# Optimization experiments

Hardware: AMD Instinct MI355X
Metric: run time of the kernel (lower is better)

The kernel has to match this reference:

```python
import jax, jax.numpy as jnp
import numpy as np

D_MODEL = 768
N_HEADS = 12
D_K = 64
EPS = 1e-5


def setup_inputs() -> dict:
    key = jax.random.key(0)
    ks = jax.random.split(key, 12)
    B, S = 4, 2048
    Q = jax.random.normal(ks[0], (B, S, D_MODEL), dtype=jnp.float32)
    K = jax.random.normal(ks[1], (B, S, D_MODEL), dtype=jnp.float32)
    V = jax.random.normal(ks[2], (B, S, D_MODEL), dtype=jnp.float32)
    attn_mask = jax.random.randint(ks[3], (B, S, S), 0, 2).astype(bool)
    s = 1.0 / np.sqrt(D_MODEL)
    Wq = jax.random.uniform(ks[4], (D_MODEL, D_MODEL), minval=-s, maxval=s)
    bq = jnp.zeros((D_MODEL,), jnp.float32)
    Wk = jax.random.uniform(ks[5], (D_MODEL, D_MODEL), minval=-s, maxval=s)
    bk = jnp.zeros((D_MODEL,), jnp.float32)
    Wv = jax.random.uniform(ks[6], (D_MODEL, D_MODEL), minval=-s, maxval=s)
    bv = jnp.zeros((D_MODEL,), jnp.float32)
    Wo = jax.random.uniform(ks[7], (D_MODEL, D_MODEL), minval=-s, maxval=s)
    bo = jnp.zeros((D_MODEL,), jnp.float32)
    gamma = jnp.ones((D_MODEL,), jnp.float32)
    beta = jnp.zeros((D_MODEL,), jnp.float32)
    return {"Q": Q, "K": K, "V": V, "attn_mask": attn_mask,
            "Wq": Wq, "bq": bq, "Wk": Wk, "bk": bk, "Wv": Wv, "bv": bv,
            "Wo": Wo, "bo": bo, "gamma": gamma, "beta": beta}


def _mha(Q, K, V, attn_mask, Wq, bq, Wk, bk, Wv, bv, Wo, bo, gamma, beta):
    B, S, _ = Q.shape
    # projections -> [B, H, S, d]
    q = (Q @ Wq + bq).reshape(B, S, N_HEADS, D_K).transpose(0, 2, 1, 3)
    k = (K @ Wk + bk).reshape(B, S, N_HEADS, D_K).transpose(0, 2, 1, 3)
    v = (V @ Wv + bv).reshape(B, S, N_HEADS, D_K).transpose(0, 2, 1, 3)
    # scaled dot-product attention with explicit [B,H,S,S] scores
    scores = jnp.einsum("bhqd,bhkd->bhqk", q, k) / np.sqrt(D_K)
    scores = jnp.where(attn_mask[:, None, :, :], -1e9, scores)
    attn = jax.nn.softmax(scores, axis=-1)
    ctx = jnp.einsum("bhqk,bhkd->bhqd", attn, v)
    ctx = ctx.transpose(0, 2, 1, 3).reshape(B, S, N_HEADS * D_K)
    out = ctx @ Wo + bo + Q  # output projection + residual
    # LayerNorm
    mu = jnp.mean(out, axis=-1, keepdims=True)
    var = jnp.mean(jnp.square(out - mu), axis=-1, keepdims=True)
    return (out - mu) * jax.lax.rsqrt(var + EPS) * gamma + beta


def reference(Q, K, V, attn_mask, Wq, bq, Wk, bk, Wv, bv, Wo, bo, gamma, beta):
    return _mha(Q, K, V, attn_mask, Wq, bq, Wk, bk, Wv, bv, Wo, bo, gamma, beta)
```

## Files before the change

kernel.cpp:

```cpp
#include <hip/hip_runtime.h>
#include <stdint.h>

#define BB 4
#define SS 2048
#define HH 12
#define DKd 64
#define DM 768
#define MROWS (BB*SS)

typedef __bf16 bfp;
typedef bfp bf16x8 __attribute__((ext_vector_type(8)));
typedef float f32x4 __attribute__((ext_vector_type(4)));

__device__ __forceinline__ unsigned short f2bf(float f) {
  union { float f; unsigned u; } c; c.f = f;
  unsigned u = c.u;
  u += 0x7FFFu + ((u >> 16) & 1u);
  return (unsigned short)(u >> 16);
}

__device__ __forceinline__ f32x4 mfma16(bf16x8 a, bf16x8 b, f32x4 c) {
  return __builtin_amdgcn_mfma_f32_16x16x32_bf16(a, b, c, 0, 0, 0);
}

__global__ __launch_bounds__(256) void wt_kernel(
    const float* __restrict__ Wq, const float* __restrict__ Wk,
    const float* __restrict__ Wv, const float* __restrict__ Wo,
    unsigned short* __restrict__ wT) {
  __shared__ float t[32][33];
  int mtx = blockIdx.z;
  const float* W = mtx == 0 ? Wq : mtx == 1 ? Wk : mtx == 2 ? Wv : Wo;
  unsigned short* out = wT + (size_t)mtx * DM * DM;
  int n0 = blockIdx.x * 32, k0 = blockIdx.y * 32;
  int tx = threadIdx.x & 31, ty = threadIdx.x >> 5;
#pragma unroll
  for (int i = 0; i < 4; i++)
    t[ty + 8 * i][tx] = W[(size_t)(k0 + ty + 8 * i) * DM + n0 + tx];
  __syncthreads();
#pragma unroll
  for (int i = 0; i < 4; i++)
    out[(size_t)(n0 + ty + 8 * i) * DM + k0 + tx] = f2bf(t[tx][ty + 8 * i]);
}

__global__ __launch_bounds__(256) void maskpack_kernel(
    const void* __restrict__ mask, unsigned short* __restrict__ pkm) {
  __shared__ int mode;
  if (threadIdx.x == 0) {
    const unsigned* w = (const unsigned*)mask;
    bool word_like = true;
    for (int i = 0; i < 64; i++) {
      unsigned x = w[i];
      if (!(x == 0u || x == 1u || x == 0x3F800000u)) { word_like = false; break; }
    }
    mode = word_like ? 1 : 0;
  }
  __syncthreads();
  int md = mode;
  int lane = threadIdx.x & 63;
  size_t total = (size_t)BB * SS * SS;
  size_t stride = (size_t)gridDim.x * blockDim.x;
  for (size_t i = (size_t)blockIdx.x * blockDim.x + threadIdx.x; i < total; i += stride) {
    int v = md ? (((const unsigned*)mask)[i] != 0u)
               : (((const unsigned char*)mask)[i] != 0);
    unsigned long long bb = __ballot(v);
    if ((lane & 15) == 0)
      pkm[i >> 4] = (unsigned short)((bb >> lane) & 0xFFFFull);
  }
}

#define Bb 128
#define LDA 40
__global__ __launch_bounds__(256) void proj_kernel(
    const float* __restrict__ Xq, const float* __restrict__ Xk, const float* __restrict__ Xv,
    const unsigned short* __restrict__ wTall,
    const float* __restrict__ bq, const float* __restrict__ bk, const float* __restrict__ bv,
    unsigned short* __restrict__ oq, unsigned short* __restrict__ ok, unsigned short* __restrict__ ov) {
  __shared__ unsigned short Al[Bb][LDA];
  __shared__ unsigned short Bl[Bb][LDA];

  int lin = blockIdx.x + gridDim.x * (blockIdx.y + gridDim.y * blockIdx.z);
  int work = (lin & 7) * 144 + (lin >> 3);
  int z = work / 384, rem = work - z * 384;
  int xb_ = rem / 6, yb = rem - xb_ * 6;

  const float* X = z == 0 ? Xq : z == 1 ? Xk : Xv;
  const unsigned short* wT = wTall + (size_t)z * DM * DM;
  const float* bias = z == 0 ? bq : z == 1 ? bk : bv;
  unsigned short* out = z == 0 ? oq : z == 1 ? ok : ov;

  int m0 = xb_ * Bb, n0 = yb * Bb;
  int tid = threadIdx.x, lane = tid & 63, wid = tid >> 6;
  int wr = (wid >> 1) * 64, wc = (wid & 1) * 64;
  int l15 = lane & 15, l4 = lane >> 4;

  f32x4 zero = {0.f, 0.f, 0.f, 0.f};
  f32x4 acc[4][4];
#pragma unroll
  for (int m = 0; m < 4; m++)
#pragma unroll
    for (int n = 0; n < 4; n++) acc[m][n] = zero;

  for (int k0 = 0; k0 < DM; k0 += 32) {
#pragma unroll
    for (int it = 0; it < 4; it++) {
      int flat = it * 256 + tid;
      int r = flat >> 3, c4 = flat & 7;
      float4 v = *reinterpret_cast<const float4*>(&X[(size_t)(m0 + r) * DM + k0 + c4 * 4]);
      unsigned short* dst = &Al[r][c4 * 4];
      dst[0] = f2bf(v.x); dst[1] = f2bf(v.y); dst[2] = f2bf(v.z); dst[3] = f2bf(v.w);
    }
#pragma unroll
    for (int it = 0; it < 2; it++) {
      int flat = it * 256 + tid;
      int r = flat >> 2, c = flat & 3;
      *reinterpret_cast<uint4*>(&Bl[r][c * 8]) =
          *reinterpret_cast<const uint4*>(&wT[(size_t)(n0 + r) * DM + k0 + c * 8]);
    }
    __syncthreads();
    bf16x8 af[4], bfr[4];
#pragma unroll
    for (int m = 0; m < 4; m++)
      af[m] = *reinterpret_cast<const bf16x8*>(&Al[wr + m * 16 + l15][l4 * 8]);
#pragma unroll
    for (int n = 0; n < 4; n++)
      bfr[n] = *reinterpret_cast<const bf16x8*>(&Bl[wc + n * 16 + l15][l4 * 8]);
#pragma unroll
    for (int m = 0; m < 4; m++)
#pragma unroll
      for (int n = 0; n < 4; n++)
        acc[m][n] = mfma16(af[m], bfr[n], acc[m][n]);
    __syncthreads();
  }
#pragma unroll
  for (int n = 0; n < 4; n++) {
    int col = n0 + wc + n * 16 + l15;
    float bv_ = bias[col];
    int h = col >> 6, d = col & 63;
#pragma unroll
    for (int m = 0; m < 4; m++) {
      int rowb = m0 + wr + m * 16 + l4 * 4;
#pragma unroll
      for (int j = 0; j < 4; j++) {
        int row = rowb + j;
        int b = row >> 11, s = row & 2047;
        out[((size_t)((b * HH + h) * SS + s)) * DKd + d] = f2bf(acc[m][n][j] + bv_);
      }
    }
  }
}

__global__ __launch_bounds__(256) void vtrans_kernel(
    const unsigned short* __restrict__ v, unsigned short* __restrict__ vT) {
  __shared__ unsigned short t[64][65];
  int bh = blockIdx.y;
  int s0 = blockIdx.x * 64;
  const unsigned short* src = v + (size_t)bh * SS * DKd;
  unsigned short* dst = vT + (size_t)bh * DKd * SS;
  int tid = threadIdx.x;
#pragma unroll
  for (int it = 0; it < 16; it++) {
    int r = it * 4 + (tid >> 6), c = tid & 63;
    t[r][c] = src[(size_t)(s0 + r) * DKd + c];
  }
  __syncthreads();
#pragma unroll
  for (int it = 0; it < 16; it++) {
    int r = it * 4 + (tid >> 6), c = tid & 63;
    dst[(size_t)r * SS + s0 + c] = t[c][r];
  }
}

#define QT 64
#define KT 64
#define LKV 72
#define LKP 76
__global__ __launch_bounds__(256) void attn_kernel(
    const unsigned short* __restrict__ q, const unsigned short* __restrict__ k,
    const unsigned short* __restrict__ vT, const unsigned short* __restrict__ pkm,
    unsigned short* __restrict__ ctx) {
  __shared__ unsigned short kl[KT][LKV];
  __shared__ unsigned short vl[DKd][LKV];
  __shared__ unsigned short pl[QT][LKP];

  int lin = blockIdx.x + blockIdx.y * gridDim.x;
  int work = (lin & 7) * 192 + (lin >> 3);
  int bh = work >> 5;
  int q0 = (work & 31) * QT;
  int b = bh / HH, h = bh - b * HH;
  int tid = threadIdx.x, lane = tid & 63, w = tid >> 6;
  int l15 = lane & 15, l4 = lane >> 4;
  const unsigned short* qp = q + (size_t)bh * SS * DKd;
  const unsigned short* kp = k + (size_t)bh * SS * DKd;
  const unsigned short* vp = vT + (size_t)bh * DKd * SS;
  const unsigned short* pkb = pkm + (size_t)b * SS * (SS / 16);

  bf16x8 aq[2];
#pragma unroll
  for (int ks = 0; ks < 2; ks++)
    aq[ks] = *reinterpret_cast<const bf16x8*>(
        &qp[(size_t)(q0 + w * 16 + l15) * DKd + ks * 32 + l4 * 8]);

  f32x4 zero = {0.f, 0.f, 0.f, 0.f};
  f32x4 acc[4];
  float lr[4] = {0.f, 0.f, 0.f, 0.f};
#pragma unroll
  for (int dn = 0; dn < 4; dn++) acc[dn] = zero;

  const float cs = 0.125f * 1.44269504f;

  for (int kt = 0; kt < SS / KT; kt++) {
#pragma unroll
    for (int it = 0; it < 2; it++) {
      int flat = it * 256 + tid;
      int r = flat >> 3, c = flat & 7;
      *reinterpret_cast<uint4*>(&kl[r][c * 8]) =
          *reinterpret_cast<const uint4*>(&kp[(size_t)(kt * KT + r) * DKd + c * 8]);
    }
#pragma unroll
    for (int it = 0; it < 2; it++) {
      int flat = it * 256 + tid;
      int r = flat >> 3, c = flat & 7;
      *reinterpret_cast<uint4*>(&vl[r][c * 8]) =
          *reinterpret_cast<const uint4*>(&vp[(size_t)r * SS + kt * KT + c * 8]);
    }
    __syncthreads();

    f32x4 sf[4];
#pragma unroll
    for (int n = 0; n < 4; n++) sf[n] = zero;
#pragma unroll
    for (int ks = 0; ks < 2; ks++) {
#pragma unroll
      for (int n = 0; n < 4; n++) {
        bf16x8 bk_ = *reinterpret_cast<const bf16x8*>(&kl[n * 16 + l15][ks * 32 + l4 * 8]);
        sf[n] = mfma16(aq[ks], bk_, sf[n]);
      }
    }

    unsigned long long pm[4];
#pragma unroll
    for (int j = 0; j < 4; j++)
      pm[j] = *reinterpret_cast<const unsigned long long*>(
          &pkb[(size_t)(q0 + w * 16 + l4 * 4 + j) * (SS / 16) + kt * 4]);
#pragma unroll
    for (int n = 0; n < 4; n++) {
#pragma unroll
      for (int j = 0; j < 4; j++) {
        unsigned bit = (unsigned)(pm[j] >> (n * 16 + l15)) & 1u;
        float arg = bit ? -1000.0f : sf[n][j] * cs;
        float p = __builtin_amdgcn_exp2f(arg);
        sf[n][j] = p;
        lr[j] += p;
      }
    }

#pragma unroll
    for (int n = 0; n < 4; n++) {
      unsigned r01, r23;
      asm("v_cvt_pk_bf16_f32 %0, %1, %2" : "=v"(r01) : "v"(sf[n][0]), "v"(sf[n][1]));
      asm("v_cvt_pk_bf16_f32 %0, %1, %2" : "=v"(r23) : "v"(sf[n][2]), "v"(sf[n][3]));
      int col = n * 16 + l15;
      pl[w * 16 + l4 * 4 + 0][col] = (unsigned short)(r01 & 0xFFFFu);
      pl[w * 16 + l4 * 4 + 1][col] = (unsigned short)(r01 >> 16);
      pl[w * 16 + l4 * 4 + 2][col] = (unsigned short)(r23 & 0xFFFFu);
      pl[w * 16 + l4 * 4 + 3][col] = (unsigned short)(r23 >> 16);
    }

    union { uint4 u; bf16x8 v; } ap[2];
#pragma unroll
    for (int ks = 0; ks < 2; ks++) {
      uint2 lo = *reinterpret_cast<const uint2*>(&pl[w * 16 + l15][ks * 32 + l4 * 8]);
      uint2 hi = *reinterpret_cast<const uint2*>(&pl[w * 16 + l15][ks * 32 + l4 * 8 + 4]);
      ap[ks].u = make_uint4(lo.x, lo.y, hi.x, hi.y);
    }

#pragma unroll
    for (int ks = 0; ks < 2; ks++) {
#pragma unroll
      for (int dn = 0; dn < 4; dn++) {
        bf16x8 bv_ = *reinterpret_cast<const bf16x8*>(&vl[dn * 16 + l15][ks * 32 + l4 * 8]);
        acc[dn] = mfma16(ap[ks].v, bv_, acc[dn]);
      }
    }
    __syncthreads();
  }

#pragma unroll
  for (int j = 0; j < 4; j++) {
#pragma unroll
    for (int off = 1; off < 16; off <<= 1) lr[j] += __shfl_xor(lr[j], off);
    lr[j] = 1.0f / lr[j];
  }
#pragma unroll
  for (int dn = 0; dn < 4; dn++) {
#pragma unroll
    for (int j = 0; j < 4; j++) {
      int grow = b * SS + q0 + w * 16 + l4 * 4 + j;
      ctx[(size_t)grow * DM + h * 64 + dn * 16 + l15] = f2bf(acc[dn][j] * lr[j]);
    }
  }
}

__global__ __launch_bounds__(256) void oproj_kernel(
    const unsigned short* __restrict__ ctx, const unsigned short* __restrict__ wT,
    const float* __restrict__ bo, const float* __restrict__ Qin, float* __restrict__ out) {
  __shared__ unsigned short Al[Bb][LDA];
  __shared__ unsigned short Bl[Bb][LDA];

  int lin = blockIdx.x + blockIdx.y * gridDim.x;
  int work = (lin & 7) * 48 + (lin >> 3);
  int xb_ = work / 6, yb = work - xb_ * 6;
  int m0 = xb_ * Bb, n0 = yb * Bb;
  int tid = threadIdx.x, lane = tid & 63, wid = tid >> 6;
  int wr = (wid >> 1) * 64, wc = (wid & 1) * 64;
  int l15 = lane & 15, l4 = lane >> 4;

  f32x4 zero = {0.f, 0.f, 0.f, 0.f};
  f32x4 acc[4][4];
#pragma unroll
  for (int m = 0; m < 4; m++)
#pragma unroll
    for (int n = 0; n < 4; n++) acc[m][n] = zero;

  for (int k0 = 0; k0 < DM; k0 += 32) {
#pragma unroll
    for (int it = 0; it < 2; it++) {
      int flat = it * 256 + tid;
      int r = flat >> 2, c = flat & 3;
      *reinterpret_cast<uint4*>(&Al[r][c * 8]) =
          *reinterpret_cast<const uint4*>(&ctx[(size_t)(m0 + r) * DM + k0 + c * 8]);
    }
#pragma unroll
    for (int it = 0; it < 2; it++) {
      int flat = it * 256 + tid;
      int r = flat >> 2, c = flat & 3;
      *reinterpret_cast<uint4*>(&Bl[r][c * 8]) =
          *reinterpret_cast<const uint4*>(&wT[(size_t)(n0 + r) * DM + k0 + c * 8]);
    }
    __syncthreads();
    bf16x8 af[4], bfr[4];
#pragma unroll
    for (int m = 0; m < 4; m++)
      af[m] = *reinterpret_cast<const bf16x8*>(&Al[wr + m * 16 + l15][l4 * 8]);
#pragma unroll
    for (int n = 0; n < 4; n++)
      bfr[n] = *reinterpret_cast<const bf16x8*>(&Bl[wc + n * 16 + l15][l4 * 8]);
#pragma unroll
    for (int m = 0; m < 4; m++)
#pragma unroll
      for (int n = 0; n < 4; n++)
        acc[m][n] = mfma16(af[m], bfr[n], acc[m][n]);
    __syncthreads();
  }
#pragma unroll
  for (int n = 0; n < 4; n++) {
    int col = n0 + wc + n * 16 + l15;
    float bv_ = bo[col];
#pragma unroll
    for (int m = 0; m < 4; m++) {
      int rowb = m0 + wr + m * 16 + l4 * 4;
#pragma unroll
      for (int j = 0; j < 4; j++) {
        int row = rowb + j;
        out[(size_t)row * DM + col] = acc[m][n][j] + bv_ + Qin[(size_t)row * DM + col];
      }
    }
  }
}

__global__ __launch_bounds__(256) void ln_kernel(
    float* __restrict__ out, const float* __restrict__ gamma, const float* __restrict__ beta) {
  int row = blockIdx.x;
  float* p = out + (size_t)row * DM;
  int t = threadIdx.x;
  float x0 = p[t], x1 = p[t + 256], x2 = p[t + 512];
  float s = x0 + x1 + x2, s2 = x0 * x0 + x1 * x1 + x2 * x2;
#pragma unroll
  for (int off = 1; off < 64; off <<= 1) {
    s += __shfl_xor(s, off);
    s2 += __shfl_xor(s2, off);
  }
  __shared__ float red[8];
  int w = t >> 6, lane = t & 63;
  if (lane == 0) { red[w] = s; red[4 + w] = s2; }
  __syncthreads();
  s = red[0] + red[1] + red[2] + red[3];
  s2 = red[4] + red[5] + red[6] + red[7];
  float mu = s * (1.0f / DM);
  float var = s2 * (1.0f / DM) - mu * mu;
  float rs = rsqrtf(var + 1e-5f);
  p[t] = (x0 - mu) * rs * gamma[t] + beta[t];
  p[t + 256] = (x1 - mu) * rs * gamma[t + 256] + beta[t + 256];
  p[t + 512] = (x2 - mu) * rs * gamma[t + 512] + beta[t + 512];
}

extern "C" void kernel_launch(void* const* d_in, const int* in_sizes, int n_in,
                              void* d_out, int out_size, void* d_ws, size_t ws_size,
                              hipStream_t stream) {
  const float* Qin = (const float*)d_in[0];
  const float* Kin = (const float*)d_in[1];
  const float* Vin = (const float*)d_in[2];
  const void* mask = d_in[3];
  const float* Wq = (const float*)d_in[4];
  const float* bq = (const float*)d_in[5];
  const float* Wk = (const float*)d_in[6];
  const float* bk = (const float*)d_in[7];
  const float* Wv = (const float*)d_in[8];
  const float* bv = (const float*)d_in[9];
  const float* Wo = (const float*)d_in[10];
  const float* bo = (const float*)d_in[11];
  const float* gamma = (const float*)d_in[12];
  const float* beta = (const float*)d_in[13];

  char* ws = (char*)d_ws;
  unsigned short* wT  = (unsigned short*)(ws);
  unsigned short* pk  = (unsigned short*)(ws + 4718592);
  unsigned short* qb  = (unsigned short*)(ws + 6815744);
  unsigned short* kb  = (unsigned short*)(ws + 6815744 + 12582912);
  unsigned short* vb  = (unsigned short*)(ws + 6815744 + 2 * 12582912);
  unsigned short* vTb = (unsigned short*)(ws + 6815744 + 3 * 12582912);
  unsigned short* ctx = vb;

  wt_kernel<<<dim3(24, 24, 4), 256, 0, stream>>>(Wq, Wk, Wv, Wo, wT);
  maskpack_kernel<<<2048, 256, 0, stream>>>(mask, pk);
  proj_kernel<<<dim3(64, 6, 3), 256, 0, stream>>>(Qin, Kin, Vin, wT, bq, bk, bv, qb, kb, vb);
  vtrans_kernel<<<dim3(32, 48), 256, 0, stream>>>(vb, vTb);
  attn_kernel<<<dim3(32, 48), 256, 0, stream>>>(qb, kb, vTb, pk, ctx);
  oproj_kernel<<<dim3(64, 6), 256, 0, stream>>>(ctx, wT + (size_t)3 * DM * DM, bo, Qin, (float*)d_out);
  ln_kernel<<<8192, 256, 0, stream>>>((float*)d_out, gamma, beta);
}
```

Baseline: 473.3 us.

## Pre-convert inputs to bf16, use direct global-to-LDS loads, widen attention key tile

Adds a conversion kernel that turns the fp32 Q/K/V activations into bf16 once, so the projection GEMM can stream bf16 tiles with global_load_lds directly into unpadded shared memory. The output projection GEMM gets the same direct-to-LDS loads. The attention kernel doubles the key tile to 128, loading wider mask words and fusing the softmax and bf16 pack loops. This costs an extra kernel launch, an extra bf16 activation buffer to write and read, and unpadded LDS rows that may cause bank conflicts.

```diff
diff --git a/kernel.cpp b/kernel.cpp
--- a/kernel.cpp
+++ b/kernel.cpp
@@ -21,6 +21,12 @@
 
 __device__ __forceinline__ f32x4 mfma16(bf16x8 a, bf16x8 b, f32x4 c) {
   return __builtin_amdgcn_mfma_f32_16x16x32_bf16(a, b, c, 0, 0, 0);
+}
+
+__device__ __forceinline__ void gload_lds16(const void* g, void* l) {
+  __builtin_amdgcn_global_load_lds(
+      (const __attribute__((address_space(1))) unsigned int*)g,
+      (__attribute__((address_space(3))) unsigned int*)l, 16, 0, 0);
 }
 
 __global__ __launch_bounds__(256) void wt_kernel(
@@ -68,22 +74,35 @@
   }
 }
 
+__global__ __launch_bounds__(256) void cvt_kernel(
+    const float* __restrict__ Q, const float* __restrict__ K, const float* __restrict__ V,
+    unsigned short* __restrict__ xb) {
+  int z = blockIdx.z;
+  const float* src = z == 0 ? Q : z == 1 ? K : V;
+  unsigned short* dst = xb + (size_t)z * MROWS * DM;
+  size_t i = ((size_t)blockIdx.x * 256 + threadIdx.x) * 4;
+  float4 v = *reinterpret_cast<const float4*>(&src[i]);
+  unsigned r01, r23;
+  asm("v_cvt_pk_bf16_f32 %0, %1, %2" : "=v"(r01) : "v"(v.x), "v"(v.y));
+  asm("v_cvt_pk_bf16_f32 %0, %1, %2" : "=v"(r23) : "v"(v.z), "v"(v.w));
+  *reinterpret_cast<uint2*>(&dst[i]) = make_uint2(r01, r23);
+}
+
 #define Bb 128
-#define LDA 40
+#define BKp 32
 __global__ __launch_bounds__(256) void proj_kernel(
-    const float* __restrict__ Xq, const float* __restrict__ Xk, const float* __restrict__ Xv,
-    const unsigned short* __restrict__ wTall,
+    const unsigned short* __restrict__ Xall, const unsigned short* __restrict__ wTall,
     const float* __restrict__ bq, const float* __restrict__ bk, const float* __restrict__ bv,
     unsigned short* __restrict__ oq, unsigned short* __restrict__ ok, unsigned short* __restrict__ ov) {
-  __shared__ unsigned short Al[Bb][LDA];
-  __shared__ unsigned short Bl[Bb][LDA];
+  __shared__ unsigned short Al[Bb][BKp];
+  __shared__ unsigned short Bl[Bb][BKp];
 
   int lin = blockIdx.x + gridDim.x * (blockIdx.y + gridDim.y * blockIdx.z);
   int work = (lin & 7) * 144 + (lin >> 3);
   int z = work / 384, rem = work - z * 384;
   int xb_ = rem / 6, yb = rem - xb_ * 6;
 
-  const float* X = z == 0 ? Xq : z == 1 ? Xk : Xv;
+  const unsigned short* X = Xall + (size_t)z * MROWS * DM;
   const unsigned short* wT = wTall + (size_t)z * DM * DM;
   const float* bias = z == 0 ? bq : z == 1 ? bk : bv;
   unsigned short* out = z == 0 ? oq : z == 1 ? ok : ov;
@@ -100,21 +119,15 @@
 #pragma unroll
     for (int n = 0; n < 4; n++) acc[m][n] = zero;
 
-  for (int k0 = 0; k0 < DM; k0 += 32) {
-#pragma unroll
-    for (int it = 0; it < 4; it++) {
-      int flat = it * 256 + tid;
-      int r = flat >> 3, c4 = flat & 7;
-      float4 v = *reinterpret_cast<const float4*>(&X[(size_t)(m0 + r) * DM + k0 + c4 * 4]);
-      unsigned short* dst = &Al[r][c4 * 4];
-      dst[0] = f2bf(v.x); dst[1] = f2bf(v.y); dst[2] = f2bf(v.z); dst[3] = f2bf(v.w);
-    }
-#pragma unroll
-    for (int it = 0; it < 2; it++) {
-      int flat = it * 256 + tid;
-      int r = flat >> 2, c = flat & 3;
-      *reinterpret_cast<uint4*>(&Bl[r][c * 8]) =
-          *reinterpret_cast<const uint4*>(&wT[(size_t)(n0 + r) * DM + k0 + c * 8]);
+  for (int k0 = 0; k0 < DM; k0 += BKp) {
+#pragma unroll
+    for (int r = 0; r < 2; ++r) {
+      int seg = r * 4 + wid;
+      int Lb = seg * 1024 + lane * 16;
+      int row = Lb >> 6;
+      int cu = (Lb & 63) >> 1;
+      gload_lds16(&X[(size_t)(m0 + row) * DM + k0 + cu], (char*)&Al[0][0] + seg * 1024);
+      gload_lds16(&wT[(size_t)(n0 + row) * DM + k0 + cu], (char*)&Bl[0][0] + seg * 1024);
     }
     __syncthreads();
     bf16x8 af[4], bfr[4];
@@ -171,15 +184,16 @@
 }
 
 #define QT 64
-#define KT 64
+#define KT 128
 #define LKV 72
-#define LKP 76
+#define LDV 136
+#define LKP 132
 __global__ __launch_bounds__(256) void attn_kernel(
     const unsigned short* __restrict__ q, const unsigned short* __restrict__ k,
     const unsigned short* __restrict__ vT, const unsigned short* __restrict__ pkm,
     unsigned short* __restrict__ ctx) {
   __shared__ unsigned short kl[KT][LKV];
-  __shared__ unsigned short vl[DKd][LKV];
+  __shared__ unsigned short vl[DKd][LDV];
   __shared__ unsigned short pl[QT][LKP];
 
   int lin = blockIdx.x + blockIdx.y * gridDim.x;
@@ -210,52 +224,52 @@
 
   for (int kt = 0; kt < SS / KT; kt++) {
 #pragma unroll
-    for (int it = 0; it < 2; it++) {
+    for (int it = 0; it < 4; it++) {
       int flat = it * 256 + tid;
       int r = flat >> 3, c = flat & 7;
       *reinterpret_cast<uint4*>(&kl[r][c * 8]) =
           *reinterpret_cast<const uint4*>(&kp[(size_t)(kt * KT + r) * DKd + c * 8]);
     }
 #pragma unroll
-    for (int it = 0; it < 2; it++) {
+    for (int it = 0; it < 4; it++) {
       int flat = it * 256 + tid;
-      int r = flat >> 3, c = flat & 7;
+      int r = flat >> 4, c = flat & 15;
       *reinterpret_cast<uint4*>(&vl[r][c * 8]) =
           *reinterpret_cast<const uint4*>(&vp[(size_t)r * SS + kt * KT + c * 8]);
     }
     __syncthreads();
 
-    f32x4 sf[4];
-#pragma unroll
-    for (int n = 0; n < 4; n++) sf[n] = zero;
+    f32x4 sf[8];
+#pragma unroll
+    for (int n = 0; n < 8; n++) sf[n] = zero;
 #pragma unroll
     for (int ks = 0; ks < 2; ks++) {
 #pragma unroll
-      for (int n = 0; n < 4; n++) {
+      for (int n = 0; n < 8; n++) {
         bf16x8 bk_ = *reinterpret_cast<const bf16x8*>(&kl[n * 16 + l15][ks * 32 + l4 * 8]);
         sf[n] = mfma16(aq[ks], bk_, sf[n]);
       }
     }
 
-    unsigned long long pm[4];
-#pragma unroll
-    for (int j = 0; j < 4; j++)
-      pm[j] = *reinterpret_cast<const unsigned long long*>(
-          &pkb[(size_t)(q0 + w * 16 + l4 * 4 + j) * (SS / 16) + kt * 4]);
-#pragma unroll
-    for (int n = 0; n < 4; n++) {
+    unsigned mw[4][4];
+#pragma unroll
+    for (int j = 0; j < 4; j++) {
+      uint4 mm = *reinterpret_cast<const uint4*>(
+          &pkb[(size_t)(q0 + w * 16 + l4 * 4 + j) * (SS / 16) + kt * 8]);
+      mw[j][0] = mm.x; mw[j][1] = mm.y; mw[j][2] = mm.z; mw[j][3] = mm.w;
+    }
+
+#pragma unroll
+    for (int n = 0; n < 8; n++) {
+      unsigned sh = (n & 1) * 16;
 #pragma unroll
       for (int j = 0; j < 4; j++) {
-        unsigned bit = (unsigned)(pm[j] >> (n * 16 + l15)) & 1u;
+        unsigned bit = (mw[j][n >> 1] >> (sh + l15)) & 1u;
         float arg = bit ? -1000.0f : sf[n][j] * cs;
         float p = __builtin_amdgcn_exp2f(arg);
         sf[n][j] = p;
         lr[j] += p;
       }
-    }
-
-#pragma unroll
-    for (int n = 0; n < 4; n++) {
       unsigned r01, r23;
       asm("v_cvt_pk_bf16_f32 %0, %1, %2" : "=v"(r01) : "v"(sf[n][0]), "v"(sf[n][1]));
       asm("v_cvt_pk_bf16_f32 %0, %1, %2" : "=v"(r23) : "v"(sf[n][2]), "v"(sf[n][3]));
@@ -266,16 +280,16 @@
       pl[w * 16 + l4 * 4 + 3][col] = (unsigned short)(r23 >> 16);
     }
 
-    union { uint4 u; bf16x8 v; } ap[2];
-#pragma unroll
-    for (int ks = 0; ks < 2; ks++) {
+    union { uint4 u; bf16x8 v; } ap[4];
+#pragma unroll
+    for (int ks = 0; ks < 4; ks++) {
       uint2 lo = *reinterpret_cast<const uint2*>(&pl[w * 16 + l15][ks * 32 + l4 * 8]);
       uint2 hi = *reinterpret_cast<const uint2*>(&pl[w * 16 + l15][ks * 32 + l4 * 8 + 4]);
       ap[ks].u = make_uint4(lo.x, lo.y, hi.x, hi.y);
     }
 
 #pragma unroll
-    for (int ks = 0; ks < 2; ks++) {
+    for (int ks = 0; ks < 4; ks++) {
 #pragma unroll
       for (int dn = 0; dn < 4; dn++) {
         bf16x8 bv_ = *reinterpret_cast<const bf16x8*>(&vl[dn * 16 + l15][ks * 32 + l4 * 8]);
@@ -304,8 +318,8 @@
 __global__ __launch_bounds__(256) void oproj_kernel(
     const unsigned short* __restrict__ ctx, const unsigned short* __restrict__ wT,
     const float* __restrict__ bo, const float* __restrict__ Qin, float* __restrict__ out) {
-  __shared__ unsigned short Al[Bb][LDA];
-  __shared__ unsigned short Bl[Bb][LDA];
+  __shared__ unsigned short Al[Bb][BKp];
+  __shared__ unsigned short Bl[Bb][BKp];
 
   int lin = blockIdx.x + blockIdx.y * gridDim.x;
   int work = (lin & 7) * 48 + (lin >> 3);
@@ -322,20 +336,15 @@
 #pragma unroll
     for (int n = 0; n < 4; n++) acc[m][n] = zero;
 
-  for (int k0 = 0; k0 < DM; k0 += 32) {
-#pragma unroll
-    for (int it = 0; it < 2; it++) {
-      int flat = it * 256 + tid;
-      int r = flat >> 2, c = flat & 3;
-      *reinterpret_cast<uint4*>(&Al[r][c * 8]) =
-          *reinterpret_cast<const uint4*>(&ctx[(size_t)(m0 + r) * DM + k0 + c * 8]);
-    }
-#pragma unroll
-    for (int it = 0; it < 2; it++) {
-      int flat = it * 256 + tid;
-      int r = flat >> 2, c = flat & 3;
-      *reinterpret_cast<uint4*>(&Bl[r][c * 8]) =
-          *reinterpret_cast<const uint4*>(&wT[(size_t)(n0 + r) * DM + k0 + c * 8]);
+  for (int k0 = 0; k0 < DM; k0 += BKp) {
+#pragma unroll
+    for (int r = 0; r < 2; ++r) {
+      int seg = r * 4 + wid;
+      int Lb = seg * 1024 + lane * 16;
+      int row = Lb >> 6;
+      int cu = (Lb & 63) >> 1;
+      gload_lds16(&ctx[(size_t)(m0 + row) * DM + k0 + cu], (char*)&Al[0][0] + seg * 1024);
+      gload_lds16(&wT[(size_t)(n0 + row) * DM + k0 + cu], (char*)&Bl[0][0] + seg * 1024);
     }
     __syncthreads();
     bf16x8 af[4], bfr[4];
@@ -415,15 +424,17 @@
   char* ws = (char*)d_ws;
   unsigned short* wT  = (unsigned short*)(ws);
   unsigned short* pk  = (unsigned short*)(ws + 4718592);
-  unsigned short* qb  = (unsigned short*)(ws + 6815744);
-  unsigned short* kb  = (unsigned short*)(ws + 6815744 + 12582912);
-  unsigned short* vb  = (unsigned short*)(ws + 6815744 + 2 * 12582912);
-  unsigned short* vTb = (unsigned short*)(ws + 6815744 + 3 * 12582912);
+  unsigned short* xbf = (unsigned short*)(ws + 6815744);
+  unsigned short* qb  = (unsigned short*)(ws + 6815744 + 37748736);
+  unsigned short* kb  = (unsigned short*)(ws + 6815744 + 37748736 + 12582912);
+  unsigned short* vb  = (unsigned short*)(ws + 6815744 + 37748736 + 2 * 12582912);
+  unsigned short* vTb = (unsigned short*)(ws + 6815744 + 37748736 + 3 * 12582912);
   unsigned short* ctx = vb;
 
   wt_kernel<<<dim3(24, 24, 4), 256, 0, stream>>>(Wq, Wk, Wv, Wo, wT);
   maskpack_kernel<<<2048, 256, 0, stream>>>(mask, pk);
-  proj_kernel<<<dim3(64, 6, 3), 256, 0, stream>>>(Qin, Kin, Vin, wT, bq, bk, bv, qb, kb, vb);
+  cvt_kernel<<<dim3(6144, 1, 3), 256, 0, stream>>>(Qin, Kin, Vin, xbf);
+  proj_kernel<<<dim3(64, 6, 3), 256, 0, stream>>>(xbf, wT, bq, bk, bv, qb, kb, vb);
   vtrans_kernel<<<dim3(32, 48), 256, 0, stream>>>(vb, vTb);
   attn_kernel<<<dim3(32, 48), 256, 0, stream>>>(qb, kb, vTb, pk, ctx);
   oproj_kernel<<<dim3(64, 6), 256, 0, stream>>>(ctx, wT + (size_t)3 * DM * DM, bo, Qin, (float*)d_out);
```

Measured after the change: 443.1 us. -6.4%, faster.
